# Kernel optimization log

Measured on AMD Instinct MI355X. Metric: run time of the kernel, lower is better.

## Reference

```python
import jax, jax.numpy as jnp
import numpy as np

S = 8          # num_syndromes (distance-3 surface code)
Q = 9          # num_qubits
F = 64         # n_node_features
H = 256        # hidden_size
ITERS = 3      # n_iters
B = 65536      # batch_size (shots)
N = B * S      # total nodes in batched graph
E = 2097152    # num edges (~avg degree 4)


def setup_inputs() -> dict:
    key = jax.random.key(0)
    ks = jax.random.split(key, 20)
    sc = 0.05
    inp = {
        "syndromes": jax.random.uniform(ks[0], (N, 1), dtype=jnp.float32),
        "edge_index": jax.random.randint(ks[1], (2, E), 0, N, dtype=jnp.int64),
        "batch_size": B,
        # embed: Linear(1, F)
        "embed_W": jax.random.normal(ks[2], (1, F), jnp.float32) * sc,
        "embed_b": jnp.zeros((F,), jnp.float32),
        # GCNConv per iter: weight (F,F) + bias (F,)
        "gcn_W": jax.random.normal(ks[3], (ITERS, F, F), jnp.float32) * sc,
        "gcn_b": jnp.zeros((ITERS, F), jnp.float32),
        # refine MLP per iter: F->H->F
        "ref_W1": jax.random.normal(ks[4], (ITERS, F, H), jnp.float32) * sc,
        "ref_b1": jnp.zeros((ITERS, H), jnp.float32),
        "ref_W2": jax.random.normal(ks[5], (ITERS, H, F), jnp.float32) * sc,
        "ref_b2": jnp.zeros((ITERS, F), jnp.float32),
        # error head per iter: F*S -> H -> H//2 -> Q
        "head_W1": jax.random.normal(ks[6], (ITERS, F * S, H), jnp.float32) * sc,
        "head_b1": jnp.zeros((ITERS, H), jnp.float32),
        "head_W2": jax.random.normal(ks[7], (ITERS, H, H // 2), jnp.float32) * sc,
        "head_b2": jnp.zeros((ITERS, H // 2), jnp.float32),
        "head_W3": jax.random.normal(ks[8], (ITERS, H // 2, Q), jnp.float32) * sc,
        "head_b3": jnp.zeros((ITERS, Q), jnp.float32),
    }
    return inp


def _gcn(x, src, dst, norm, W, b, n_nodes):
    # x' = D^{-1/2} (A+I) D^{-1/2} (x W) + b   (PyG GCNConv, eval mode)
    xw = x @ W                                  # [N, F]
    msg = xw[src] * norm[:, None]               # gather + edge-normalize
    out = jax.ops.segment_sum(msg, dst, num_segments=n_nodes)
    return out + b


def reference(syndromes, edge_index, batch_size,
              embed_W, embed_b, gcn_W, gcn_b,
              ref_W1, ref_b1, ref_W2, ref_b2,
              head_W1, head_b1, head_W2, head_b2, head_W3, head_b3):
    n_nodes = syndromes.shape[0]
    loops = jnp.arange(n_nodes, dtype=edge_index.dtype)
    src = jnp.concatenate([edge_index[0], loops])
    dst = jnp.concatenate([edge_index[1], loops])
    deg = jnp.zeros((n_nodes,), syndromes.dtype).at[dst].add(1.0)
    dinv = 1.0 / jnp.sqrt(deg)                  # deg >= 1 due to self-loops
    norm = dinv[src] * dinv[dst]

    h = syndromes @ embed_W + embed_b           # [N, F]
    outs = []
    for i in range(ITERS):
        h = _gcn(h, src, dst, norm, gcn_W[i], gcn_b[i], n_nodes)
        h = jax.nn.relu(h)
        r = jax.nn.relu(h @ ref_W1[i] + ref_b1[i]) @ ref_W2[i] + ref_b2[i]
        h = jax.nn.relu(h + r)
        h_all = h.reshape(batch_size, -1)        # [B, S*F]
        z = jax.nn.relu(h_all @ head_W1[i] + head_b1[i])
        z = jax.nn.relu(z @ head_W2[i] + head_b2[i])
        outs.append(jax.nn.sigmoid(z @ head_W3[i] + head_b3[i]))  # [B, Q]
    return tuple(outs)
```

## Files before the change

### kernel.cpp

```cpp
#include <hip/hip_runtime.h>
#include <cstdint>

#define NN 524288
#define NB 65536
#define NQ 9
#define NEDGE 2097152
#define NITERS 3

typedef __attribute__((ext_vector_type(8))) short bf16x8;
typedef __attribute__((ext_vector_type(4))) float f32x4;

__device__ __forceinline__ unsigned short f2b(float f) {
    union { float f; unsigned u; } v; v.f = f;
    unsigned u = v.u;
    u += 0x7FFFu + ((u >> 16) & 1u);
    return (unsigned short)(u >> 16);
}
__device__ __forceinline__ float b2f(unsigned short b) {
    union { unsigned u; float f; } v; v.u = ((unsigned)b) << 16;
    return v.f;
}
__device__ __forceinline__ float frelu(float v) { return v > 0.f ? v : 0.f; }

__device__ __forceinline__ int sw64(int r, int c)  { return r * 64  + (c ^ ((r & 7) << 3)); }


__global__ void k_cnt_init(int* __restrict__ cnt) {
    cnt[blockIdx.x * 256 + threadIdx.x] = 0;
}

__global__ void k_hist(const int* __restrict__ eidx, int* __restrict__ cnt) {
    int e = blockIdx.x * 256 + threadIdx.x;
    atomicAdd(&cnt[eidx[NEDGE + e]], 1);
}

__global__ void k_scan1(const int* __restrict__ cnt, int* __restrict__ rowptr,
                        int* __restrict__ bsum, float* __restrict__ dinv) {
    __shared__ int sd[256];
    int tid = threadIdx.x;
    int base = (blockIdx.x * 256 + tid) * 4;
    int c0 = cnt[base], c1 = cnt[base + 1], c2 = cnt[base + 2], c3 = cnt[base + 3];
    dinv[base]     = rsqrtf(1.f + (float)c0);
    dinv[base + 1] = rsqrtf(1.f + (float)c1);
    dinv[base + 2] = rsqrtf(1.f + (float)c2);
    dinv[base + 3] = rsqrtf(1.f + (float)c3);
    int t = c0 + c1 + c2 + c3;
    sd[tid] = t; __syncthreads();
    for (int o = 1; o < 256; o <<= 1) {
        int v = (tid >= o) ? sd[tid - o] : 0;
        __syncthreads();
        sd[tid] += v;
        __syncthreads();
    }
    int excl = sd[tid] - t;
    rowptr[base]     = excl;
    rowptr[base + 1] = excl + c0;
    rowptr[base + 2] = excl + c0 + c1;
    rowptr[base + 3] = excl + c0 + c1 + c2;
    if (tid == 255) bsum[blockIdx.x] = sd[255];
}

__global__ void k_scan2(int* __restrict__ bsum) {
    __shared__ int sd[512];
    int tid = threadIdx.x;
    int v = bsum[tid];
    sd[tid] = v; __syncthreads();
    for (int o = 1; o < 512; o <<= 1) {
        int u = (tid >= o) ? sd[tid - o] : 0;
        __syncthreads();
        sd[tid] += u;
        __syncthreads();
    }
    bsum[tid] = sd[tid] - v;
}

__global__ void k_scan3(int* __restrict__ rowptr, const int* __restrict__ bsum,
                        int* __restrict__ cursor) {
    int tid = threadIdx.x;
    int base = (blockIdx.x * 256 + tid) * 4;
    int off = bsum[blockIdx.x];
#pragma unroll
    for (int j = 0; j < 4; ++j) {
        int r = rowptr[base + j] + off;
        rowptr[base + j] = r;
        cursor[base + j] = r;
    }
    if (blockIdx.x == 511 && tid == 255) rowptr[NN] = NEDGE;
}

__global__ void k_fill(const int* __restrict__ eidx, int* __restrict__ cursor,
                       int* __restrict__ srcs) {
    int e = blockIdx.x * 256 + threadIdx.x;
    int s = eidx[e], d = eidx[NEDGE + e];
    int pos = atomicAdd(&cursor[d], 1);
    srcs[pos] = s;
}

__global__ void k_trans(const float* __restrict__ W, unsigned short* __restrict__ Wt,
                        int K, int M, int total) {
    int o = blockIdx.x * 256 + threadIdx.x;
    if (o >= total) return;
    int km = K * M;
    int it = o / km;
    int rem = o - it * km;
    int m = rem / K;
    int k = rem - m * K;
    Wt[o] = f2b(W[(size_t)it * km + (size_t)k * M + m]);
}



template<bool EMBED>
__global__ __launch_bounds__(256, 6) void k_gcnref(
    const int* __restrict__ rowptr, const int* __restrict__ srcs,
    const float* __restrict__ dinv,
    const float* __restrict__ syn, const float* __restrict__ embW,
    const float* __restrict__ embB,
    const unsigned short* __restrict__ hin,
    const unsigned short* __restrict__ Wgt, const float* __restrict__ bg,
    const unsigned short* __restrict__ W1t, const float* __restrict__ b1,
    const unsigned short* __restrict__ W2t, const float* __restrict__ b2,
    unsigned short* __restrict__ hout)
{
    __shared__ unsigned short tl[64 * 64];
    __shared__ unsigned short zl[64 * 64];
    const int tid = threadIdx.x, wid = tid >> 6, l = tid & 63;
    const int lr = l & 15, lkq = l >> 4;
    const int g = l >> 4, i = l & 15;
    const int rowBase = blockIdx.x * 64;
    const int nb = rowBase + wid * 16;

    float4 ew4, eb4;
    if (EMBED) {
        ew4 = *(const float4*)(embW + i * 4);
        eb4 = *(const float4*)(embB + i * 4);
    }

    for (int q = 0; q < 4; ++q) {
        const int node = nb + q * 4 + g;
        int beg = rowptr[node];
        int deg = rowptr[node + 1] - beg;
        int   sl = (i < deg) ? srcs[beg + i] : node;
        float wl = (i < deg) ? dinv[sl] : 0.f;

        float dn = dinv[node];
        float a0, a1, a2, a3;
        if (EMBED) {
            float s0 = syn[node];
            a0 = (s0 * ew4.x + eb4.x) * dn;
            a1 = (s0 * ew4.y + eb4.y) * dn;
            a2 = (s0 * ew4.z + eb4.z) * dn;
            a3 = (s0 * ew4.w + eb4.w) * dn;
        } else {
            ushort4 sv = *(const ushort4*)(hin + (size_t)node * 64 + i * 4);
            a0 = b2f(sv.x) * dn; a1 = b2f(sv.y) * dn;
            a2 = b2f(sv.z) * dn; a3 = b2f(sv.w) * dn;
        }

        int dmax = max(max(__shfl(deg, 0), __shfl(deg, 16)),
                       max(__shfl(deg, 32), __shfl(deg, 48)));
        int dfast = dmax < 16 ? dmax : 16;

        for (int p = 0; p < dfast; p += 8) {
            int   s[8]; float w[8];
#pragma unroll
            for (int u = 0; u < 8; ++u) {
                int idx = (l & 48) + p + u;
                s[u] = __shfl(sl, idx);
                w[u] = __shfl(wl, idx);
            }
            if (EMBED) {
                float sy[8];
#pragma unroll
                for (int u = 0; u < 8; ++u) sy[u] = syn[s[u]];
#pragma unroll
                for (int u = 0; u < 8; ++u) {
                    a0 += (sy[u] * ew4.x + eb4.x) * w[u];
                    a1 += (sy[u] * ew4.y + eb4.y) * w[u];
                    a2 += (sy[u] * ew4.z + eb4.z) * w[u];
                    a3 += (sy[u] * ew4.w + eb4.w) * w[u];
                }
            } else {
                ushort4 v[8];
#pragma unroll
                for (int u = 0; u < 8; ++u)
                    v[u] = *(const ushort4*)(hin + (size_t)s[u] * 64 + i * 4);
#pragma unroll
                for (int u = 0; u < 8; ++u) {
                    a0 += b2f(v[u].x) * w[u];
                    a1 += b2f(v[u].y) * w[u];
                    a2 += b2f(v[u].z) * w[u];
                    a3 += b2f(v[u].w) * w[u];
                }
            }
        }
        if (deg > 16) {
            for (int t = 16; t < deg; ++t) {
                int st = srcs[beg + t];
                float wt = dinv[st];
                if (EMBED) {
                    float sy = syn[st];
                    a0 += (sy * ew4.x + eb4.x) * wt;
                    a1 += (sy * ew4.y + eb4.y) * wt;
                    a2 += (sy * ew4.z + eb4.z) * wt;
                    a3 += (sy * ew4.w + eb4.w) * wt;
                } else {
                    ushort4 v = *(const ushort4*)(hin + (size_t)st * 64 + i * 4);
                    a0 += b2f(v.x) * wt; a1 += b2f(v.y) * wt;
                    a2 += b2f(v.z) * wt; a3 += b2f(v.w) * wt;
                }
            }
        }
        ushort4 o;
        o.x = f2b(a0 * dn); o.y = f2b(a1 * dn);
        o.z = f2b(a2 * dn); o.w = f2b(a3 * dn);
        *(ushort4*)&tl[sw64(wid * 16 + q * 4 + g, i * 4)] = o;
    }

    f32x4 ag[4];
#pragma unroll
    for (int mg = 0; mg < 4; ++mg) ag[mg] = (f32x4){0.f, 0.f, 0.f, 0.f};
#pragma unroll
    for (int kc = 0; kc < 64; kc += 32) {
        bf16x8 bfr = *(const bf16x8*)&tl[sw64(wid * 16 + lr, kc + lkq * 8)];
#pragma unroll
        for (int mg = 0; mg < 4; ++mg) {
            bf16x8 a = *(const bf16x8*)(Wgt + (size_t)(mg * 16 + lr) * 64 + kc + lkq * 8);
            ag[mg] = __builtin_amdgcn_mfma_f32_16x16x32_bf16(a, bfr, ag[mg], 0, 0, 0);
        }
    }
#pragma unroll
    for (int mg = 0; mg < 4; ++mg) {
        int m0 = mg * 16 + lkq * 4;
        float4 bb = *(const float4*)(bg + m0);
        ushort4 o;
        o.x = f2b(frelu(ag[mg][0] + bb.x));
        o.y = f2b(frelu(ag[mg][1] + bb.y));
        o.z = f2b(frelu(ag[mg][2] + bb.z));
        o.w = f2b(frelu(ag[mg][3] + bb.w));
        *(ushort4*)&tl[sw64(wid * 16 + lr, m0)] = o;
    }
    __syncthreads();

    f32x4 r2[4];
#pragma unroll
    for (int mg = 0; mg < 4; ++mg) r2[mg] = (f32x4){0.f, 0.f, 0.f, 0.f};

#pragma unroll
    for (int qt = 0; qt < 4; ++qt) {
        f32x4 z1a[4];
#pragma unroll
        for (int ng = 0; ng < 4; ++ng) z1a[ng] = (f32x4){0.f, 0.f, 0.f, 0.f};
#pragma unroll
        for (int kc = 0; kc < 64; kc += 32) {
            bf16x8 a = *(const bf16x8*)(W1t +
                (size_t)(qt * 64 + wid * 16 + lr) * 64 + kc + lkq * 8);
#pragma unroll
            for (int ng = 0; ng < 4; ++ng) {
                bf16x8 bfr = *(const bf16x8*)&tl[sw64(ng * 16 + lr, kc + lkq * 8)];
                z1a[ng] = __builtin_amdgcn_mfma_f32_16x16x32_bf16(a, bfr, z1a[ng], 0, 0, 0);
            }
        }
        {
            int m0 = wid * 16 + lkq * 4;
            float4 bb = *(const float4*)(b1 + qt * 64 + m0);
#pragma unroll
            for (int ng = 0; ng < 4; ++ng) {
                int n = ng * 16 + lr;
                ushort4 o;
                o.x = f2b(frelu(z1a[ng][0] + bb.x));
                o.y = f2b(frelu(z1a[ng][1] + bb.y));
                o.z = f2b(frelu(z1a[ng][2] + bb.z));
                o.w = f2b(frelu(z1a[ng][3] + bb.w));
                *(ushort4*)&zl[sw64(n, m0)] = o;
            }
        }
        __syncthreads();

#pragma unroll
        for (int kc = 0; kc < 64; kc += 32) {
            bf16x8 bz = *(const bf16x8*)&zl[sw64(wid * 16 + lr, kc + lkq * 8)];
#pragma unroll
            for (int mg = 0; mg < 4; ++mg) {
                bf16x8 a = *(const bf16x8*)(W2t +
                    (size_t)(mg * 16 + lr) * 256 + qt * 64 + kc + lkq * 8);
                r2[mg] = __builtin_amdgcn_mfma_f32_16x16x32_bf16(a, bz, r2[mg], 0, 0, 0);
            }
        }
        if (qt < 3) __syncthreads();
    }

    {
        int n = wid * 16 + lr;
#pragma unroll
        for (int mg = 0; mg < 4; ++mg) {
            int m0 = mg * 16 + lkq * 4;
            float4 bb = *(const float4*)(b2 + m0);
            ushort4 rs = *(const ushort4*)&tl[sw64(n, m0)];
            ushort4 o;
            o.x = f2b(frelu(r2[mg][0] + bb.x + b2f(rs.x)));
            o.y = f2b(frelu(r2[mg][1] + bb.y + b2f(rs.y)));
            o.z = f2b(frelu(r2[mg][2] + bb.z + b2f(rs.z)));
            o.w = f2b(frelu(r2[mg][3] + bb.w + b2f(rs.w)));
            *(ushort4*)&tl[sw64(n, m0)] = o;
        }
    }
    __syncthreads();
    {
        int r = tid >> 2, c16 = (tid & 3) * 16;
        bf16x8 v0 = *(const bf16x8*)&tl[sw64(r, c16)];
        bf16x8 v1 = *(const bf16x8*)&tl[sw64(r, c16 + 8)];
        *(bf16x8*)(hout + (size_t)(rowBase + r) * 64 + c16) = v0;
        *(bf16x8*)(hout + (size_t)(rowBase + r) * 64 + c16 + 8) = v1;
    }
}

__global__ __launch_bounds__(256) void k_head(const unsigned short* __restrict__ hb,
                                              const unsigned short* __restrict__ W1t,
                                              const float* __restrict__ b1,
                                              const unsigned short* __restrict__ W2t,
                                              const float* __restrict__ b2,
                                              const unsigned short* __restrict__ W3t,
                                              const float* __restrict__ b3,
                                              float* __restrict__ out) {
    __shared__ unsigned short z1[64][280];
    __shared__ unsigned short z2[64][152];
    const int tid = threadIdx.x, wid = tid >> 6, l = tid & 63;
    const int lr = l & 15, lkq = l >> 4;
    const unsigned short* hall = hb + (size_t)blockIdx.x * 64 * 512;

    f32x4 acc1[4][4];
#pragma unroll
    for (int mg = 0; mg < 4; ++mg)
#pragma unroll
        for (int ng = 0; ng < 4; ++ng) acc1[mg][ng] = (f32x4){0.f, 0.f, 0.f, 0.f};

    for (int kc = 0; kc < 512; kc += 32) {
        bf16x8 bfr[4];
#pragma unroll
        for (int ng = 0; ng < 4; ++ng)
            bfr[ng] = *(const bf16x8*)(hall + (size_t)(ng * 16 + lr) * 512 + kc + lkq * 8);
#pragma unroll
        for (int mg = 0; mg < 4; ++mg) {
            bf16x8 a = *(const bf16x8*)(W1t + (size_t)(wid * 64 + mg * 16 + lr) * 512 + kc + lkq * 8);
#pragma unroll
            for (int ng = 0; ng < 4; ++ng)
                acc1[mg][ng] = __builtin_amdgcn_mfma_f32_16x16x32_bf16(a, bfr[ng], acc1[mg][ng], 0, 0, 0);
        }
    }
#pragma unroll
    for (int mg = 0; mg < 4; ++mg) {
        int m0 = wid * 64 + mg * 16 + lkq * 4;
        float4 bb = *(const float4*)(b1 + m0);
#pragma unroll
        for (int ng = 0; ng < 4; ++ng) {
            int n = ng * 16 + lr;
            ushort4 o;
            o.x = f2b(frelu(acc1[mg][ng][0] + bb.x));
            o.y = f2b(frelu(acc1[mg][ng][1] + bb.y));
            o.z = f2b(frelu(acc1[mg][ng][2] + bb.z));
            o.w = f2b(frelu(acc1[mg][ng][3] + bb.w));
            *(ushort4*)&z1[n][m0] = o;
        }
    }
    __syncthreads();

    f32x4 acc2[2][4];
#pragma unroll
    for (int mg = 0; mg < 2; ++mg)
#pragma unroll
        for (int ng = 0; ng < 4; ++ng) acc2[mg][ng] = (f32x4){0.f, 0.f, 0.f, 0.f};
#pragma unroll
    for (int kc = 0; kc < 256; kc += 32) {
        bf16x8 bfr[4];
#pragma unroll
        for (int ng = 0; ng < 4; ++ng)
            bfr[ng] = *(const bf16x8*)&z1[ng * 16 + lr][kc + lkq * 8];
#pragma unroll
        for (int mg = 0; mg < 2; ++mg) {
            bf16x8 a = *(const bf16x8*)(W2t + (size_t)(wid * 32 + mg * 16 + lr) * 256 + kc + lkq * 8);
#pragma unroll
            for (int ng = 0; ng < 4; ++ng)
                acc2[mg][ng] = __builtin_amdgcn_mfma_f32_16x16x32_bf16(a, bfr[ng], acc2[mg][ng], 0, 0, 0);
        }
    }
#pragma unroll
    for (int mg = 0; mg < 2; ++mg) {
        int m0 = wid * 32 + mg * 16 + lkq * 4;
        float4 bb = *(const float4*)(b2 + m0);
#pragma unroll
        for (int ng = 0; ng < 4; ++ng) {
            int n = ng * 16 + lr;
            ushort4 o;
            o.x = f2b(frelu(acc2[mg][ng][0] + bb.x));
            o.y = f2b(frelu(acc2[mg][ng][1] + bb.y));
            o.z = f2b(frelu(acc2[mg][ng][2] + bb.z));
            o.w = f2b(frelu(acc2[mg][ng][3] + bb.w));
            *(ushort4*)&z2[n][m0] = o;
        }
    }
    __syncthreads();

    f32x4 acc3 = (f32x4){0.f, 0.f, 0.f, 0.f};
    int arow = lr < 9 ? lr : 8;
#pragma unroll
    for (int kc = 0; kc < 128; kc += 32) {
        bf16x8 bz = *(const bf16x8*)&z2[wid * 16 + lr][kc + lkq * 8];
        bf16x8 a = *(const bf16x8*)(W3t + (size_t)arow * 128 + kc + lkq * 8);
        acc3 = __builtin_amdgcn_mfma_f32_16x16x32_bf16(a, bz, acc3, 0, 0, 0);
    }
    {
        long shot = (long)blockIdx.x * 64 + wid * 16 + lr;
#pragma unroll
        for (int r = 0; r < 4; ++r) {
            int m = lkq * 4 + r;
            if (m < 9) {
                float v = acc3[r] + b3[m];
                out[shot * 9 + m] = 1.f / (1.f + expf(-v));
            }
        }
    }
}


extern "C" void kernel_launch(void* const* d_in, const int* in_sizes, int n_in,
                              void* d_out, int out_size, void* d_ws, size_t ws_size,
                              hipStream_t stream) {
    const float* syn  = (const float*)d_in[0];
    const int*   eidx = (const int*)d_in[1];
    const float* embW = (const float*)d_in[3];
    const float* embB = (const float*)d_in[4];
    const float* gcnW = (const float*)d_in[5];
    const float* gcnB = (const float*)d_in[6];
    const float* rW1  = (const float*)d_in[7];
    const float* rB1  = (const float*)d_in[8];
    const float* rW2  = (const float*)d_in[9];
    const float* rB2  = (const float*)d_in[10];
    const float* hW1  = (const float*)d_in[11];
    const float* hB1  = (const float*)d_in[12];
    const float* hW2  = (const float*)d_in[13];
    const float* hB2  = (const float*)d_in[14];
    const float* hW3  = (const float*)d_in[15];
    const float* hB3  = (const float*)d_in[16];
    float* out = (float*)d_out;

    unsigned short* h0     = (unsigned short*)d_ws;
    unsigned short* h1     = h0 + (size_t)NN * 64;
    int*            srcs   = (int*)(h1 + (size_t)NN * 64);
    int*            rowptr = srcs + NEDGE;
    int*            cnt    = rowptr + NN + 256;
    int*            bsum   = cnt + NN;
    float*          dinv   = (float*)(bsum + 512);
    unsigned short* gcnWt  = (unsigned short*)(dinv + NN);
    unsigned short* rW1t   = gcnWt + 3 * 64 * 64;
    unsigned short* rW2t   = rW1t + 3 * 64 * 256;
    unsigned short* hW1t   = rW2t + 3 * 256 * 64;
    unsigned short* hW2t   = hW1t + 3 * 512 * 256;
    unsigned short* hW3t   = hW2t + 3 * 256 * 128;

    k_trans<<<(3*64*64   + 255)/256, 256, 0, stream>>>(gcnW, gcnWt, 64, 64,  3*64*64);
    k_trans<<<(3*64*256  + 255)/256, 256, 0, stream>>>(rW1,  rW1t,  64, 256, 3*64*256);
    k_trans<<<(3*256*64  + 255)/256, 256, 0, stream>>>(rW2,  rW2t,  256, 64, 3*256*64);
    k_trans<<<(3*512*256 + 255)/256, 256, 0, stream>>>(hW1,  hW1t,  512, 256, 3*512*256);
    k_trans<<<(3*256*128 + 255)/256, 256, 0, stream>>>(hW2,  hW2t,  256, 128, 3*256*128);
    k_trans<<<(3*128*9   + 255)/256, 256, 0, stream>>>(hW3,  hW3t,  128, 9,   3*128*9);

    k_cnt_init<<<NN / 256, 256, 0, stream>>>(cnt);
    k_hist<<<NEDGE / 256, 256, 0, stream>>>(eidx, cnt);
    k_scan1<<<512, 256, 0, stream>>>(cnt, rowptr, bsum, dinv);
    k_scan2<<<1, 512, 0, stream>>>(bsum);
    k_scan3<<<512, 256, 0, stream>>>(rowptr, bsum, cnt);
    k_fill<<<NEDGE / 256, 256, 0, stream>>>(eidx, cnt, srcs);

    unsigned short* hcur = h0;
    unsigned short* hnxt = h1;
    for (int i = 0; i < NITERS; ++i) {
        unsigned short* hdst = (i == 0) ? h0 : hnxt;
        if (i == 0) {
            k_gcnref<true><<<NN / 64, 256, 0, stream>>>(
                rowptr, srcs, dinv, syn, embW, embB, nullptr,
                gcnWt, gcnB,
                rW1t, rB1, rW2t, rB2, h0);
        } else {
            k_gcnref<false><<<NN / 64, 256, 0, stream>>>(
                rowptr, srcs, dinv, nullptr, nullptr, nullptr, hcur,
                gcnWt + (size_t)i * 64 * 64, gcnB + (size_t)i * 64,
                rW1t + (size_t)i * 64 * 256, rB1 + (size_t)i * 256,
                rW2t + (size_t)i * 256 * 64, rB2 + (size_t)i * 64, hdst);
        }
        k_head<<<NB / 64, 256, 0, stream>>>(hdst,
                                            hW1t + (size_t)i * 512 * 256, hB1 + (size_t)i * 256,
                                            hW2t + (size_t)i * 256 * 128, hB2 + (size_t)i * 128,
                                            hW3t + (size_t)i * 128 * 9,   hB3 + (size_t)i * 9,
                                            out + (size_t)i * NB * NQ);
        if (i == 0) { hcur = h0; hnxt = h1; }
        else { unsigned short* t = hcur; hcur = hdst; hnxt = t; }
    }
}
```

Measured before the change: 1.217 ms.

## Merge weight transposes, reuse swizzled LDS in head kernel, nontemporal CSR fill

Replaces six weight-transpose launches with a single kernel that dispatches on the output index. In the head kernel, the two padded LDS buffers become one XOR-swizzled buffer reused for both layers, with an added barrier before the reuse, and launch bounds now request 4 blocks per SM. The CSR fill writes source indices with nontemporal stores. The aim is to cut launch overhead and LDS footprint so more head blocks fit per CU, at the cost of an extra barrier and possible register pressure from the occupancy hint.

```diff
diff --git a/kernel.cpp b/kernel.cpp
--- a/kernel.cpp
+++ b/kernel.cpp
@@ -23,6 +23,8 @@
 __device__ __forceinline__ float frelu(float v) { return v > 0.f ? v : 0.f; }
 
 __device__ __forceinline__ int sw64(int r, int c)  { return r * 64  + (c ^ ((r & 7) << 3)); }
+__device__ __forceinline__ int sw128(int r, int c) { return r * 128 + (c ^ ((r & 7) << 3)); }
+__device__ __forceinline__ int sw256(int r, int c) { return r * 256 + (c ^ ((r & 7) << 3)); }
 
 
 __global__ void k_cnt_init(int* __restrict__ cnt) {
@@ -93,19 +95,31 @@
     int e = blockIdx.x * 256 + threadIdx.x;
     int s = eidx[e], d = eidx[NEDGE + e];
     int pos = atomicAdd(&cursor[d], 1);
-    srcs[pos] = s;
-}
-
-__global__ void k_trans(const float* __restrict__ W, unsigned short* __restrict__ Wt,
-                        int K, int M, int total) {
+    __builtin_nontemporal_store(s, &srcs[pos]);
+}
+
+__global__ void k_trans_all(const float* __restrict__ gcnW, const float* __restrict__ rW1,
+                            const float* __restrict__ rW2, const float* __restrict__ hW1,
+                            const float* __restrict__ hW2, const float* __restrict__ hW3,
+                            unsigned short* __restrict__ gcnWt, unsigned short* __restrict__ rW1t,
+                            unsigned short* __restrict__ rW2t, unsigned short* __restrict__ hW1t,
+                            unsigned short* __restrict__ hW2t, unsigned short* __restrict__ hW3t) {
     int o = blockIdx.x * 256 + threadIdx.x;
-    if (o >= total) return;
+    const float* W; unsigned short* Wt; int K, M, base;
+    if      (o < 12288)  { W = gcnW; Wt = gcnWt; K = 64;  M = 64;  base = 0; }
+    else if (o < 61440)  { W = rW1;  Wt = rW1t;  K = 64;  M = 256; base = 12288; }
+    else if (o < 110592) { W = rW2;  Wt = rW2t;  K = 256; M = 64;  base = 61440; }
+    else if (o < 503808) { W = hW1;  Wt = hW1t;  K = 512; M = 256; base = 110592; }
+    else if (o < 602112) { W = hW2;  Wt = hW2t;  K = 256; M = 128; base = 503808; }
+    else if (o < 605568) { W = hW3;  Wt = hW3t;  K = 128; M = 9;   base = 602112; }
+    else return;
+    int rel = o - base;
     int km = K * M;
-    int it = o / km;
-    int rem = o - it * km;
+    int it = rel / km;
+    int rem = rel - it * km;
     int m = rem / K;
     int k = rem - m * K;
-    Wt[o] = f2b(W[(size_t)it * km + (size_t)k * M + m]);
+    Wt[rel] = f2b(W[(size_t)it * km + (size_t)k * M + m]);
 }
 
 
@@ -315,16 +329,17 @@
     }
 }
 
-__global__ __launch_bounds__(256) void k_head(const unsigned short* __restrict__ hb,
-                                              const unsigned short* __restrict__ W1t,
-                                              const float* __restrict__ b1,
-                                              const unsigned short* __restrict__ W2t,
-                                              const float* __restrict__ b2,
-                                              const unsigned short* __restrict__ W3t,
-                                              const float* __restrict__ b3,
-                                              float* __restrict__ out) {
-    __shared__ unsigned short z1[64][280];
-    __shared__ unsigned short z2[64][152];
+__global__ __launch_bounds__(256, 4) void k_head(
+    const unsigned short* __restrict__ hb,
+    const unsigned short* __restrict__ W1t,
+    const float* __restrict__ b1,
+    const unsigned short* __restrict__ W2t,
+    const float* __restrict__ b2,
+    const unsigned short* __restrict__ W3t,
+    const float* __restrict__ b3,
+    float* __restrict__ out)
+{
+    __shared__ unsigned short sm[64 * 256];
     const int tid = threadIdx.x, wid = tid >> 6, l = tid & 63;
     const int lr = l & 15, lkq = l >> 4;
     const unsigned short* hall = hb + (size_t)blockIdx.x * 64 * 512;
@@ -360,7 +375,7 @@
             o.y = f2b(frelu(acc1[mg][ng][1] + bb.y));
             o.z = f2b(frelu(acc1[mg][ng][2] + bb.z));
             o.w = f2b(frelu(acc1[mg][ng][3] + bb.w));
-            *(ushort4*)&z1[n][m0] = o;
+            *(ushort4*)&sm[sw256(n, m0)] = o;
         }
     }
     __syncthreads();
@@ -375,7 +390,7 @@
         bf16x8 bfr[4];
 #pragma unroll
         for (int ng = 0; ng < 4; ++ng)
-            bfr[ng] = *(const bf16x8*)&z1[ng * 16 + lr][kc + lkq * 8];
+            bfr[ng] = *(const bf16x8*)&sm[sw256(ng * 16 + lr, kc + lkq * 8)];
 #pragma unroll
         for (int mg = 0; mg < 2; ++mg) {
             bf16x8 a = *(const bf16x8*)(W2t + (size_t)(wid * 32 + mg * 16 + lr) * 256 + kc + lkq * 8);
@@ -384,6 +399,8 @@
                 acc2[mg][ng] = __builtin_amdgcn_mfma_f32_16x16x32_bf16(a, bfr[ng], acc2[mg][ng], 0, 0, 0);
         }
     }
+    __syncthreads();
+
 #pragma unroll
     for (int mg = 0; mg < 2; ++mg) {
         int m0 = wid * 32 + mg * 16 + lkq * 4;
@@ -396,28 +413,25 @@
             o.y = f2b(frelu(acc2[mg][ng][1] + bb.y));
             o.z = f2b(frelu(acc2[mg][ng][2] + bb.z));
             o.w = f2b(frelu(acc2[mg][ng][3] + bb.w));
-            *(ushort4*)&z2[n][m0] = o;
+            *(ushort4*)&sm[sw128(n, m0)] = o;
         }
     }
     __syncthreads();
 
-    f32x4 acc3 = (f32x4){0.f, 0.f, 0.f, 0.f};
+    f32x4 a3 = (f32x4){0.f, 0.f, 0.f, 0.f};
     int arow = lr < 9 ? lr : 8;
 #pragma unroll
     for (int kc = 0; kc < 128; kc += 32) {
-        bf16x8 bz = *(const bf16x8*)&z2[wid * 16 + lr][kc + lkq * 8];
+        bf16x8 bz = *(const bf16x8*)&sm[sw128(wid * 16 + lr, kc + lkq * 8)];
         bf16x8 a = *(const bf16x8*)(W3t + (size_t)arow * 128 + kc + lkq * 8);
-        acc3 = __builtin_amdgcn_mfma_f32_16x16x32_bf16(a, bz, acc3, 0, 0, 0);
+        a3 = __builtin_amdgcn_mfma_f32_16x16x32_bf16(a, bz, a3, 0, 0, 0);
     }
     {
         long shot = (long)blockIdx.x * 64 + wid * 16 + lr;
 #pragma unroll
         for (int r = 0; r < 4; ++r) {
             int m = lkq * 4 + r;
-            if (m < 9) {
-                float v = acc3[r] + b3[m];
-                out[shot * 9 + m] = 1.f / (1.f + expf(-v));
-            }
+            if (m < 9) out[shot * 9 + m] = 1.f / (1.f + expf(-(a3[r] + b3[m])));
         }
     }
 }
@@ -458,12 +472,8 @@
     unsigned short* hW2t   = hW1t + 3 * 512 * 256;
     unsigned short* hW3t   = hW2t + 3 * 256 * 128;
 
-    k_trans<<<(3*64*64   + 255)/256, 256, 0, stream>>>(gcnW, gcnWt, 64, 64,  3*64*64);
-    k_trans<<<(3*64*256  + 255)/256, 256, 0, stream>>>(rW1,  rW1t,  64, 256, 3*64*256);
-    k_trans<<<(3*256*64  + 255)/256, 256, 0, stream>>>(rW2,  rW2t,  256, 64, 3*256*64);
-    k_trans<<<(3*512*256 + 255)/256, 256, 0, stream>>>(hW1,  hW1t,  512, 256, 3*512*256);
-    k_trans<<<(3*256*128 + 255)/256, 256, 0, stream>>>(hW2,  hW2t,  256, 128, 3*256*128);
-    k_trans<<<(3*128*9   + 255)/256, 256, 0, stream>>>(hW3,  hW3t,  128, 9,   3*128*9);
+    k_trans_all<<<(605568 + 255) / 256, 256, 0, stream>>>(
+        gcnW, rW1, rW2, hW1, hW2, hW3, gcnWt, rW1t, rW2t, hW1t, hW2t, hW3t);
 
     k_cnt_init<<<NN / 256, 256, 0, stream>>>(cnt);
     k_hist<<<NEDGE / 256, 256, 0, stream>>>(eidx, cnt);
@@ -488,11 +498,12 @@
                 rW1t + (size_t)i * 64 * 256, rB1 + (size_t)i * 256,
                 rW2t + (size_t)i * 256 * 64, rB2 + (size_t)i * 64, hdst);
         }
-        k_head<<<NB / 64, 256, 0, stream>>>(hdst,
-                                            hW1t + (size_t)i * 512 * 256, hB1 + (size_t)i * 256,
-                                            hW2t + (size_t)i * 256 * 128, hB2 + (size_t)i * 128,
-                                            hW3t + (size_t)i * 128 * 9,   hB3 + (size_t)i * 9,
-                                            out + (size_t)i * NB * NQ);
+        k_head<<<NB / 64, 256, 0, stream>>>(
+            hdst,
+            hW1t + (size_t)i * 512 * 256, hB1 + (size_t)i * 256,
+            hW2t + (size_t)i * 256 * 128, hB2 + (size_t)i * 128,
+            hW3t + (size_t)i * 128 * 9,   hB3 + (size_t)i * 9,
+            out + (size_t)i * NB * NQ);
         if (i == 0) { hcur = h0; hnxt = h1; }
         else { unsigned short* t = hcur; hcur = hdst; hnxt = t; }
     }
```

Result: no change. 1.229 ms (+1.0%).
